# Performance work log

Measured on AMD Instinct MI355X. Metric: run time of the kernel, lower is better.

Reference implementation:

```python
import jax, jax.numpy as jnp
import numpy as np
import math

C = 256
N_HEAD = 8
GROUPS = 32
EPS = 1e-5


def group_norm(x, scale, bias, groups=GROUPS, eps=EPS):
    # x: [B, C, H, W]
    b, c, h, w = x.shape
    xg = x.reshape(b, groups, c // groups, h, w)
    mean = xg.mean(axis=(2, 3, 4), keepdims=True)
    var = xg.var(axis=(2, 3, 4), keepdims=True)
    xg = (xg - mean) * jax.lax.rsqrt(var + eps)
    x = xg.reshape(b, c, h, w)
    return x * scale[None, :, None, None] + bias[None, :, None, None]


def setup_inputs() -> dict:
    key = jax.random.key(0)
    ks = jax.random.split(key, 8)
    B, H, W = 8, 32, 32
    inp = {
        "input_q": jax.random.normal(ks[0], (B, C, H, W), dtype=jnp.float32),
        "input_kv": jax.random.normal(ks[1], (B, C, H, W), dtype=jnp.float32),
        # GroupNorm affine params (torch default: weight=1, bias=0)
        "gq_scale": jnp.ones((C,), jnp.float32),
        "gq_bias": jnp.zeros((C,), jnp.float32),
        "gkv_scale": jnp.ones((C,), jnp.float32),
        "gkv_bias": jnp.zeros((C,), jnp.float32),
        # 1x1 convs as [out, in] matrices
        "Wq": jax.random.normal(ks[2], (C, C), dtype=jnp.float32) / math.sqrt(C),
        "Wkv": jax.random.normal(ks[3], (2 * C, C), dtype=jnp.float32) / math.sqrt(C),
        "Wout": jax.random.normal(ks[4], (C, C), dtype=jnp.float32) / math.sqrt(C),
        "bout": jnp.zeros((C,), jnp.float32),
    }
    return inp


def reference(input_q, input_kv, gq_scale, gq_bias, gkv_scale, gkv_bias, Wq, Wkv, Wout, bout):
    b, c, h, w = input_q.shape
    n = N_HEAD
    d = c // n

    norm_q = group_norm(input_q, gq_scale, gq_bias)
    query = jnp.einsum('oc,bchw->bohw', Wq, norm_q).reshape(b, n, d, h, w)

    norm_kv = group_norm(input_kv, gkv_scale, gkv_bias)
    kv = jnp.einsum('oc,bchw->bohw', Wkv, norm_kv).reshape(b, n, 2 * d, h, w)
    key, value = kv[:, :, :d], kv[:, :, d:]

    attn = jnp.einsum('bnchw,bncyx->bnhwyx', query, key) / math.sqrt(c)
    attn = jax.nn.softmax(attn.reshape(b, n, h, w, h * w), axis=-1)
    attn = attn.reshape(b, n, h, w, h, w)

    out = jnp.einsum('bnhwyx,bncyx->bnchw', attn, value).reshape(b, c, h, w)
    out = jnp.einsum('oc,bchw->bohw', Wout, out) + bout[None, :, None, None]
    return out + input_q
```

## Files before the change

### kernel.cpp

```cpp
#include <hip/hip_runtime.h>
#include <hip/hip_bf16.h>
#include <math.h>
#include <string.h>

#define NB 8
#define NC 256
#define HWSZ 1024
#define NHEAD 8
#define DHEAD 32
#define NGRP 32
#define CPG 8
#define EPSV 1e-5f

typedef float f32x4 __attribute__((ext_vector_type(4)));
typedef short bf16x8 __attribute__((ext_vector_type(8)));

__device__ __forceinline__ unsigned pk2(float a, float b) {
    __hip_bfloat162 h = __float22bfloat162_rn(make_float2(a, b));
    unsigned r;
    memcpy(&r, &h, sizeof(r));
    return r;
}
__device__ __forceinline__ unsigned pk2t(float a, float b) {
    unsigned ua = __float_as_uint(a), ub = __float_as_uint(b);
    return (ua >> 16) | (ub & 0xFFFF0000u);
}
__device__ __forceinline__ unsigned short f2bf(float x) {
    __hip_bfloat16 h = __float2bfloat16(x);
    unsigned short r;
    memcpy(&r, &h, sizeof(r));
    return r;
}
__device__ __forceinline__ float ex2(float x) { return __builtin_amdgcn_exp2f(x); }

__device__ __forceinline__ void gload_lds16(const void* g, void* l) {
    __builtin_amdgcn_global_load_lds(
        (const __attribute__((address_space(1))) unsigned int*)g,
        (__attribute__((address_space(3))) unsigned int*)l, 16, 0, 0);
}

__global__ void prep_kernel(const float* __restrict__ xq,
                            const float* __restrict__ xkv,
                            const float* __restrict__ gq_scale,
                            const float* __restrict__ gq_bias,
                            const float* __restrict__ gkv_scale,
                            const float* __restrict__ gkv_bias,
                            const float* __restrict__ Wq,
                            const float* __restrict__ Wkv,
                            const float* __restrict__ Wout,
                            unsigned short* __restrict__ xnq,
                            unsigned short* __restrict__ xnkv,
                            unsigned short* __restrict__ wqb,
                            unsigned short* __restrict__ wkvb,
                            unsigned short* __restrict__ woutb) {
    if (blockIdx.x < 512) {
        int idx = blockIdx.x;
        int which = idx >> 8;
        int b = (idx >> 5) & 7;
        int g = idx & 31;
        const float* x = which ? xkv : xq;
        const float4* xb = (const float4*)(x + ((size_t)(b * NC + g * CPG)) * HWSZ);
        float s = 0.f, ss = 0.f;
        for (int i = threadIdx.x; i < (CPG * HWSZ) / 4; i += 256) {
            float4 v = xb[i];
            s += v.x + v.y + v.z + v.w;
            ss += v.x * v.x + v.y * v.y + v.z * v.z + v.w * v.w;
        }
        #pragma unroll
        for (int off = 32; off > 0; off >>= 1) {
            s += __shfl_down(s, off);
            ss += __shfl_down(ss, off);
        }
        __shared__ float red[10];
        int wid = threadIdx.x >> 6;
        if ((threadIdx.x & 63) == 0) { red[wid * 2] = s; red[wid * 2 + 1] = ss; }
        __syncthreads();
        if (threadIdx.x == 0) {
            float S = red[0] + red[2] + red[4] + red[6];
            float SS = red[1] + red[3] + red[5] + red[7];
            float mean = S * (1.f / (CPG * HWSZ));
            float var = SS * (1.f / (CPG * HWSZ)) - mean * mean;
            red[8] = mean;
            red[9] = rsqrtf(var + EPSV);
        }
        __syncthreads();
        const float mean = red[8], rstd = red[9];
        const float* scp = which ? gkv_scale : gq_scale;
        const float* bip = which ? gkv_bias : gq_bias;
        float a[8], bb[8];
        #pragma unroll
        for (int u = 0; u < 8; ++u) {
            int c = g * 8 + u;
            a[u] = rstd * scp[c];
            bb[u] = bip[c] - mean * a[u];
        }
        const int p0 = threadIdx.x * 4;
        f32x4 rowv[8];
        #pragma unroll
        for (int u = 0; u < 8; ++u)
            rowv[u] = *(const f32x4*)&x[((size_t)(b * NC + g * 8 + u)) * HWSZ + p0];
        unsigned short* xt = (which ? xnkv : xnq)
                           + (((size_t)b * NGRP + g) * HWSZ) * 8;
        #pragma unroll
        for (int pi = 0; pi < 4; ++pi) {
            uint4 o;
            o.x = pk2(rowv[0][pi] * a[0] + bb[0], rowv[1][pi] * a[1] + bb[1]);
            o.y = pk2(rowv[2][pi] * a[2] + bb[2], rowv[3][pi] * a[3] + bb[3]);
            o.z = pk2(rowv[4][pi] * a[4] + bb[4], rowv[5][pi] * a[5] + bb[5]);
            o.w = pk2(rowv[6][pi] * a[6] + bb[6], rowv[7][pi] * a[7] + bb[7]);
            *(uint4*)&xt[(size_t)(p0 + pi) * 8] = o;
        }
    } else {
        int gid = (blockIdx.x - 512) * 256 + threadIdx.x;
        int i0 = gid * 8;
        const float* src; unsigned short* dst; int off; float sc = 1.f;
        if (i0 < 65536)       { src = Wq;   dst = wqb;   off = i0;          sc = 0.0625f * 1.44269504088896f; }
        else if (i0 < 196608) { src = Wkv;  dst = wkvb;  off = i0 - 65536; }
        else                  { src = Wout; dst = woutb; off = i0 - 196608; }
        float4 v0 = *(const float4*)&src[off];
        float4 v1 = *(const float4*)&src[off + 4];
        uint4 o;
        o.x = pk2(v0.x * sc, v0.y * sc); o.y = pk2(v0.z * sc, v0.w * sc);
        o.z = pk2(v1.x * sc, v1.y * sc); o.w = pk2(v1.z * sc, v1.w * sc);
        *(uint4*)&dst[off] = o;
    }
}

__global__ __launch_bounds__(256) void qkv_gemm_kernel(
        const unsigned short* __restrict__ wqb,
        const unsigned short* __restrict__ wkvb,
        const unsigned short* __restrict__ xnq,
        const unsigned short* __restrict__ xnkv,
        unsigned short* __restrict__ qbuf,
        unsigned short* __restrict__ kbuf,
        unsigned short* __restrict__ vbuf) {
    __shared__ unsigned short Bs[64 * 256];
    const int tid = threadIdx.x;
    const int l16 = tid & 15, g = (tid >> 4) & 3, w = tid >> 6;
    const int y = blockIdx.y;
    const bool isQ = y < 4;
    const int o0 = (isQ ? y : y - 4) * 64;
    const size_t prow0 = (size_t)blockIdx.x * 64;
    const int b = (int)(prow0 >> 10);
    const int pp = (int)(prow0 & 1023);

    const unsigned short* Asrc = (isQ ? wqb : wkvb)
                               + ((size_t)o0 + 16 * w + l16) * NC;
    bf16x8 af[8];
    #pragma unroll
    for (int kk = 0; kk < 8; ++kk)
        af[kk] = *(const bf16x8*)&Asrc[(kk * 4 + g) << 3];

    const unsigned short* Xn = (isQ ? xnq : xnkv) + (size_t)b * NGRP * HWSZ * 8;
    const int prow = tid & 63, gu0 = tid >> 6;
    #pragma unroll
    for (int i = 0; i < 8; ++i) {
        int gu = gu0 + i * 4;
        uint4 v = *(const uint4*)&Xn[((size_t)gu * HWSZ + pp + prow) * 8];
        int ds = prow * 256 + ((gu ^ (prow & 7)) << 3);
        *(uint4*)&Bs[ds] = v;
    }
    __syncthreads();

    f32x4 acc[4] = {};
    const int asw = l16 & 7;
    #pragma unroll
    for (int kk = 0; kk < 8; ++kk) {
        const int koff = ((kk * 4 + g) ^ asw) << 3;
        #pragma unroll
        for (int j = 0; j < 4; ++j) {
            bf16x8 bfr = *(const bf16x8*)&Bs[(j * 16 + l16) * 256 + koff];
            acc[j] = __builtin_amdgcn_mfma_f32_16x16x32_bf16(af[kk], bfr, acc[j], 0, 0, 0);
        }
    }

    if (isQ) {
        int ob_ = o0 + 16 * w + 4 * g;
        int n = ob_ >> 5, d0 = ob_ & 31;
        unsigned short* dst = qbuf + ((size_t)(b * NHEAD + n) * HWSZ) * DHEAD + d0;
        #pragma unroll
        for (int j = 0; j < 4; ++j) {
            int p = pp + 16 * j + l16;
            uint2 st2;
            st2.x = pk2(acc[j][0], acc[j][1]);
            st2.y = pk2(acc[j][2], acc[j][3]);
            *(uint2*)&dst[(size_t)p * DHEAD] = st2;
        }
    } else {
        int n = o0 >> 6;
        int d0 = 16 * (w & 1) + 4 * g;
        if (w < 2) {
            unsigned short* dst = kbuf + ((size_t)(b * NHEAD + n) * HWSZ) * DHEAD + d0;
            #pragma unroll
            for (int j = 0; j < 4; ++j) {
                int p = pp + 16 * j + l16;
                uint2 st2;
                st2.x = pk2(acc[j][0], acc[j][1]);
                st2.y = pk2(acc[j][2], acc[j][3]);
                *(uint2*)&dst[(size_t)p * DHEAD] = st2;
            }
        } else {
            unsigned short* dst = vbuf + ((size_t)(b * NHEAD + n) * DHEAD + d0) * HWSZ;
            #pragma unroll
            for (int j = 0; j < 4; ++j) {
                int slot = ((l16 >> 2) << 3) + ((j & 1) << 2) + (l16 & 3);
                int p = pp + 32 * (j >> 1) + slot;
                #pragma unroll
                for (int r = 0; r < 4; ++r)
                    dst[(size_t)r * HWSZ + p] = f2bf(acc[j][r]);
            }
        }
    }
}

__global__ __launch_bounds__(256) void out_gemm_kernel(
        const unsigned short* __restrict__ Abase,
        const unsigned short* __restrict__ Bbase,
        const float* __restrict__ bias_out,
        const float* __restrict__ resid,
        float* __restrict__ out0) {
    __shared__ unsigned short Bs[64 * 256];
    const int tid = threadIdx.x;
    const int l16 = tid & 15, g = (tid >> 4) & 3, w = tid >> 6;
    const int o0 = blockIdx.y * 64;
    const size_t prow0 = (size_t)blockIdx.x * 64;

    const unsigned short* Asrc = Abase + (prow0 + 16 * w + l16) * NC;
    bf16x8 af[8];
    #pragma unroll
    for (int kk = 0; kk < 8; ++kk)
        af[kk] = *(const bf16x8*)&Asrc[(kk * 4 + g) << 3];

    const unsigned short* Bsrc = Bbase + (size_t)o0 * NC;
    #pragma unroll
    for (int it = 0; it < 4; ++it) {
        int idx = tid + it * 256;
        int row = idx >> 4, seg = idx & 15;
        #pragma unroll
        for (int h = 0; h < 2; ++h) {
            int sg = seg * 2 + h;
            int ds = row * 256 + ((sg ^ (row & 7)) << 3);
            *(uint4*)&Bs[ds] = *(const uint4*)&Bsrc[(size_t)row * NC + sg * 8];
        }
    }
    __syncthreads();

    f32x4 acc[4] = {};
    const int asw = l16 & 7;
    #pragma unroll
    for (int kk = 0; kk < 8; ++kk) {
        const int koff = ((kk * 4 + g) ^ asw) << 3;
        #pragma unroll
        for (int j = 0; j < 4; ++j) {
            bf16x8 b = *(const bf16x8*)&Bs[(j * 16 + l16) * 256 + koff];
            acc[j] = __builtin_amdgcn_mfma_f32_16x16x32_bf16(af[kk], b, acc[j], 0, 0, 0);
        }
    }
    const int b = (int)(prow0 >> 10);
    const int pp = (int)(prow0 & 1023);
    int p_b = pp + 16 * w + 4 * g;
    #pragma unroll
    for (int j = 0; j < 4; ++j) {
        int o = o0 + 16 * j + l16;
        float bo = bias_out[o];
        size_t off = ((size_t)b * NC + o) * HWSZ + p_b;
        float4 rs = *(const float4*)&resid[off];
        float4 vst = make_float4(acc[j][0] + bo + rs.x, acc[j][1] + bo + rs.y,
                                 acc[j][2] + bo + rs.z, acc[j][3] + bo + rs.w);
        *(float4*)&out0[off] = vst;
    }
}

__global__ __launch_bounds__(256) void attn_mfma_kernel(
        const unsigned short* __restrict__ qb,
        const unsigned short* __restrict__ kb,
        const unsigned short* __restrict__ vb,
        unsigned short* __restrict__ ob) {
    __shared__ unsigned short KV[3][4096];
    const int tid = threadIdx.x;
    const int w = tid >> 6, lane = tid & 63;
    const int l16 = lane & 15, g = lane >> 4;
    const int F = blockIdx.y * 16 + blockIdx.x;
    const int bn = (F & 7) * 8 + (F >> 7);
    const int qblk = (F >> 3) & 15;
    const int qp = qblk * 64 + w * 16 + l16;

    bf16x8 qf = *(const bf16x8*)(qb + ((size_t)bn * HWSZ + qp) * DHEAD + g * 8);

    const int kr = tid >> 2, ks = tid & 3;
    const unsigned short* ksrc = kb + (size_t)bn * HWSZ * DHEAD
                               + (size_t)kr * DHEAD + ((ks ^ (kr & 3)) << 3);
    const int vr = tid >> 3, vs = tid & 7;
    const unsigned short* vsrc = vb + (size_t)bn * DHEAD * HWSZ
                               + (size_t)vr * HWSZ + ((vs ^ (vr & 7)) << 3);
    unsigned short* lk = &KV[0][0] + w * 512;
    unsigned short* lv = &KV[0][2048] + w * 512;

#define STAGE(t) do {                                                        \
        int b3_ = (t) % 3; int ti_ = (t) & 15;                               \
        gload_lds16(ksrc + (size_t)ti_ * 64 * DHEAD, lk + b3_ * 4096);       \
        gload_lds16(vsrc + (size_t)ti_ * 64,         lv + b3_ * 4096);       \
    } while (0)

    f32x4 acc0 = {0.f, 0.f, 0.f, 0.f}, acc1 = {0.f, 0.f, 0.f, 0.f};
    f32x4 accl = {0.f, 0.f, 0.f, 0.f};
    const f32x4 z = {0.f, 0.f, 0.f, 0.f};

    const unsigned on2 = 0x3F803F80u;
    uint4 onev = make_uint4(on2, on2, on2, on2);
    bf16x8 ones;
    memcpy(&ones, &onev, sizeof(ones));

    const int ksw  = (g ^ (l16 & 3)) << 3;
    const int vsw0 = ((g)     ^ (l16 & 7)) << 3;
    const int vsw1 = ((4 + g) ^ (l16 & 7)) << 3;

    STAGE(0);
    STAGE(1);

    #pragma unroll
    for (int t = 0; t < 16; ++t) {
        const int cur = t % 3;
        asm volatile("s_waitcnt vmcnt(2)" ::: "memory");
        __builtin_amdgcn_s_barrier();
        STAGE(t + 2);

        const unsigned short* Kb = &KV[cur][0];
        const unsigned short* Vb = &KV[cur][2048];
        bf16x8 ka0 = *(const bf16x8*)&Kb[(l16)      * 32 + ksw];
        bf16x8 ka1 = *(const bf16x8*)&Kb[(16 + l16) * 32 + ksw];
        bf16x8 ka2 = *(const bf16x8*)&Kb[(32 + l16) * 32 + ksw];
        bf16x8 ka3 = *(const bf16x8*)&Kb[(48 + l16) * 32 + ksw];

        __builtin_amdgcn_s_setprio(1);
        f32x4 s0 = __builtin_amdgcn_mfma_f32_16x16x32_bf16(ka0, qf, z, 0, 0, 0);
        f32x4 s1 = __builtin_amdgcn_mfma_f32_16x16x32_bf16(ka1, qf, z, 0, 0, 0);
        f32x4 s2 = __builtin_amdgcn_mfma_f32_16x16x32_bf16(ka2, qf, z, 0, 0, 0);
        f32x4 s3 = __builtin_amdgcn_mfma_f32_16x16x32_bf16(ka3, qf, z, 0, 0, 0);
        __builtin_amdgcn_s_setprio(0);

        float p00 = ex2(s0[0]), p01 = ex2(s0[1]);
        float p02 = ex2(s0[2]), p03 = ex2(s0[3]);
        float p10 = ex2(s1[0]), p11 = ex2(s1[1]);
        float p12 = ex2(s1[2]), p13 = ex2(s1[3]);
        float p20 = ex2(s2[0]), p21 = ex2(s2[1]);
        float p22 = ex2(s2[2]), p23 = ex2(s2[3]);
        float p30 = ex2(s3[0]), p31 = ex2(s3[1]);
        float p32 = ex2(s3[2]), p33 = ex2(s3[3]);

        uint4 pwa, pwb;
        pwa.x = pk2t(p00, p01); pwa.y = pk2t(p02, p03);
        pwa.z = pk2t(p10, p11); pwa.w = pk2t(p12, p13);
        pwb.x = pk2t(p20, p21); pwb.y = pk2t(p22, p23);
        pwb.z = pk2t(p30, p31); pwb.w = pk2t(p32, p33);
        bf16x8 pf0, pf1;
        memcpy(&pf0, &pwa, sizeof(pf0));
        memcpy(&pf1, &pwb, sizeof(pf1));

        bf16x8 va0 = *(const bf16x8*)&Vb[(l16)      * 64 + vsw0];
        bf16x8 va1 = *(const bf16x8*)&Vb[(l16)      * 64 + vsw1];
        bf16x8 vb0 = *(const bf16x8*)&Vb[(16 + l16) * 64 + vsw0];
        bf16x8 vb1 = *(const bf16x8*)&Vb[(16 + l16) * 64 + vsw1];

        __builtin_amdgcn_s_setprio(1);
        acc0 = __builtin_amdgcn_mfma_f32_16x16x32_bf16(va0, pf0, acc0, 0, 0, 0);
        acc0 = __builtin_amdgcn_mfma_f32_16x16x32_bf16(va1, pf1, acc0, 0, 0, 0);
        acc1 = __builtin_amdgcn_mfma_f32_16x16x32_bf16(vb0, pf0, acc1, 0, 0, 0);
        acc1 = __builtin_amdgcn_mfma_f32_16x16x32_bf16(vb1, pf1, acc1, 0, 0, 0);
        accl = __builtin_amdgcn_mfma_f32_16x16x32_bf16(ones, pf0, accl, 0, 0, 0);
        accl = __builtin_amdgcn_mfma_f32_16x16x32_bf16(ones, pf1, accl, 0, 0, 0);
        __builtin_amdgcn_s_setprio(0);
    }
#undef STAGE

    float invl = 1.f / accl[0];

    const int b = bn >> 3, n = bn & 7;
    unsigned short* dst = ob + ((size_t)b * HWSZ + qp) * NC + n * DHEAD;
    uint2 st0, st1;
    st0.x = pk2(acc0[0] * invl, acc0[1] * invl);
    st0.y = pk2(acc0[2] * invl, acc0[3] * invl);
    st1.x = pk2(acc1[0] * invl, acc1[1] * invl);
    st1.y = pk2(acc1[2] * invl, acc1[3] * invl);
    *(uint2*)&dst[4 * g]      = st0;
    *(uint2*)&dst[16 + 4 * g] = st1;
}

extern "C" void kernel_launch(void* const* d_in, const int* in_sizes, int n_in,
                              void* d_out, int out_size, void* d_ws, size_t ws_size,
                              hipStream_t stream) {
    const float* input_q  = (const float*)d_in[0];
    const float* input_kv = (const float*)d_in[1];
    const float* gq_scale = (const float*)d_in[2];
    const float* gq_bias  = (const float*)d_in[3];
    const float* gkv_scale = (const float*)d_in[4];
    const float* gkv_bias  = (const float*)d_in[5];
    const float* Wq   = (const float*)d_in[6];
    const float* Wkv  = (const float*)d_in[7];
    const float* Wout = (const float*)d_in[8];
    const float* bout = (const float*)d_in[9];
    float* out = (float*)d_out;

    char* ws = (char*)d_ws;
    unsigned short* wqb   = (unsigned short*)(ws + 16384);
    unsigned short* wkvb  = (unsigned short*)(ws + 16384 + 131072);
    unsigned short* woutb = (unsigned short*)(ws + 16384 + 131072 + 262144);
    const size_t MB = 1024 * 1024;
    unsigned short* xnq  = (unsigned short*)(ws + 1 * MB);
    unsigned short* xnkv = (unsigned short*)(ws + 5 * MB);
    unsigned short* qbuf = (unsigned short*)(ws + 9 * MB);
    unsigned short* kbuf = (unsigned short*)(ws + 13 * MB);
    unsigned short* vbuf = (unsigned short*)(ws + 17 * MB);
    unsigned short* obuf = (unsigned short*)(ws + 21 * MB);

    prep_kernel<<<640, 256, 0, stream>>>(
        input_q, input_kv, gq_scale, gq_bias, gkv_scale, gkv_bias,
        Wq, Wkv, Wout, xnq, xnkv, wqb, wkvb, woutb);
    qkv_gemm_kernel<<<dim3(128, 12), 256, 0, stream>>>(
        wqb, wkvb, xnq, xnkv, qbuf, kbuf, vbuf);
    attn_mfma_kernel<<<dim3(16, 64), 256, 0, stream>>>(qbuf, kbuf, vbuf, obuf);
    out_gemm_kernel<<<dim3(128, 4), 256, 0, stream>>>(obuf, woutb, bout, input_q, out);
}
```

Baseline: 48.20 us.

## Switch attention kernel to 32x32x16 MFMA tiles with 128 queries per block

Rewrites the attention inner loop to use 32x32x16 bf16 MFMA instructions instead of 16x16x32. Each wave now handles 32 queries, each block 128, and the grid is halved. The K/V LDS layouts change to match the new operand fragments, and the V store order in the QKV GEMM is permuted to fit. The aim is to reuse each K/V tile across more queries and cut per-tile instruction overhead, at the cost of larger accumulators (more registers) and fewer blocks. The XOR swizzle is dropped, which may bring LDS bank conflicts.

```diff
diff --git a/kernel.cpp b/kernel.cpp
--- a/kernel.cpp
+++ b/kernel.cpp
@@ -13,6 +13,7 @@
 #define EPSV 1e-5f
 
 typedef float f32x4 __attribute__((ext_vector_type(4)));
+typedef float f32x16 __attribute__((ext_vector_type(16)));
 typedef short bf16x8 __attribute__((ext_vector_type(8)));
 
 __device__ __forceinline__ unsigned pk2(float a, float b) {
@@ -201,10 +202,10 @@
             }
         } else {
             unsigned short* dst = vbuf + ((size_t)(b * NHEAD + n) * DHEAD + d0) * HWSZ;
+            int slot = (l16 & 3) | ((l16 & 4) << 1) | ((l16 & 8) >> 1);
             #pragma unroll
             for (int j = 0; j < 4; ++j) {
-                int slot = ((l16 >> 2) << 3) + ((j & 1) << 2) + (l16 & 3);
-                int p = pp + 32 * (j >> 1) + slot;
+                int p = pp + 16 * j + slot;
                 #pragma unroll
                 for (int r = 0; r < 4; ++r)
                     dst[(size_t)r * HWSZ + p] = f2bf(acc[j][r]);
@@ -279,20 +280,21 @@
     __shared__ unsigned short KV[3][4096];
     const int tid = threadIdx.x;
     const int w = tid >> 6, lane = tid & 63;
-    const int l16 = lane & 15, g = lane >> 4;
-    const int F = blockIdx.y * 16 + blockIdx.x;
-    const int bn = (F & 7) * 8 + (F >> 7);
-    const int qblk = (F >> 3) & 15;
-    const int qp = qblk * 64 + w * 16 + l16;
-
-    bf16x8 qf = *(const bf16x8*)(qb + ((size_t)bn * HWSZ + qp) * DHEAD + g * 8);
-
-    const int kr = tid >> 2, ks = tid & 3;
+    const int l31 = lane & 31, h = lane >> 5;
+    const int F = blockIdx.y * 8 + blockIdx.x;
+    const int bn = (F & 7) * 8 + ((F >> 3) & 7);
+    const int qblk = F >> 6;
+    const int qp = qblk * 128 + w * 32 + l31;
+
+    const unsigned short* qsrc = qb + ((size_t)bn * HWSZ + qp) * DHEAD + h * 8;
+    bf16x8 qf0 = *(const bf16x8*)qsrc;
+    bf16x8 qf1 = *(const bf16x8*)(qsrc + 16);
+
     const unsigned short* ksrc = kb + (size_t)bn * HWSZ * DHEAD
-                               + (size_t)kr * DHEAD + ((ks ^ (kr & 3)) << 3);
-    const int vr = tid >> 3, vs = tid & 7;
+                               + (size_t)lane * DHEAD + w * 8;
+    const int vku = tid >> 5, vd = tid & 31;
     const unsigned short* vsrc = vb + (size_t)bn * DHEAD * HWSZ
-                               + (size_t)vr * HWSZ + ((vs ^ (vr & 7)) << 3);
+                               + (size_t)vd * HWSZ + vku * 8;
     unsigned short* lk = &KV[0][0] + w * 512;
     unsigned short* lv = &KV[0][2048] + w * 512;
 
@@ -302,18 +304,14 @@
         gload_lds16(vsrc + (size_t)ti_ * 64,         lv + b3_ * 4096);       \
     } while (0)
 
-    f32x4 acc0 = {0.f, 0.f, 0.f, 0.f}, acc1 = {0.f, 0.f, 0.f, 0.f};
-    f32x4 accl = {0.f, 0.f, 0.f, 0.f};
-    const f32x4 z = {0.f, 0.f, 0.f, 0.f};
+    f32x16 accO = {};
+    f32x16 accl = {};
+    const f32x16 z16 = {};
 
     const unsigned on2 = 0x3F803F80u;
     uint4 onev = make_uint4(on2, on2, on2, on2);
     bf16x8 ones;
     memcpy(&ones, &onev, sizeof(ones));
-
-    const int ksw  = (g ^ (l16 & 3)) << 3;
-    const int vsw0 = ((g)     ^ (l16 & 7)) << 3;
-    const int vsw1 = ((4 + g) ^ (l16 & 7)) << 3;
 
     STAGE(0);
     STAGE(1);
@@ -327,63 +325,58 @@
 
         const unsigned short* Kb = &KV[cur][0];
         const unsigned short* Vb = &KV[cur][2048];
-        bf16x8 ka0 = *(const bf16x8*)&Kb[(l16)      * 32 + ksw];
-        bf16x8 ka1 = *(const bf16x8*)&Kb[(16 + l16) * 32 + ksw];
-        bf16x8 ka2 = *(const bf16x8*)&Kb[(32 + l16) * 32 + ksw];
-        bf16x8 ka3 = *(const bf16x8*)&Kb[(48 + l16) * 32 + ksw];
-
-        __builtin_amdgcn_s_setprio(1);
-        f32x4 s0 = __builtin_amdgcn_mfma_f32_16x16x32_bf16(ka0, qf, z, 0, 0, 0);
-        f32x4 s1 = __builtin_amdgcn_mfma_f32_16x16x32_bf16(ka1, qf, z, 0, 0, 0);
-        f32x4 s2 = __builtin_amdgcn_mfma_f32_16x16x32_bf16(ka2, qf, z, 0, 0, 0);
-        f32x4 s3 = __builtin_amdgcn_mfma_f32_16x16x32_bf16(ka3, qf, z, 0, 0, 0);
-        __builtin_amdgcn_s_setprio(0);
-
-        float p00 = ex2(s0[0]), p01 = ex2(s0[1]);
-        float p02 = ex2(s0[2]), p03 = ex2(s0[3]);
-        float p10 = ex2(s1[0]), p11 = ex2(s1[1]);
-        float p12 = ex2(s1[2]), p13 = ex2(s1[3]);
-        float p20 = ex2(s2[0]), p21 = ex2(s2[1]);
-        float p22 = ex2(s2[2]), p23 = ex2(s2[3]);
-        float p30 = ex2(s3[0]), p31 = ex2(s3[1]);
-        float p32 = ex2(s3[2]), p33 = ex2(s3[3]);
-
-        uint4 pwa, pwb;
-        pwa.x = pk2t(p00, p01); pwa.y = pk2t(p02, p03);
-        pwa.z = pk2t(p10, p11); pwa.w = pk2t(p12, p13);
-        pwb.x = pk2t(p20, p21); pwb.y = pk2t(p22, p23);
-        pwb.z = pk2t(p30, p31); pwb.w = pk2t(p32, p33);
-        bf16x8 pf0, pf1;
-        memcpy(&pf0, &pwa, sizeof(pf0));
-        memcpy(&pf1, &pwb, sizeof(pf1));
-
-        bf16x8 va0 = *(const bf16x8*)&Vb[(l16)      * 64 + vsw0];
-        bf16x8 va1 = *(const bf16x8*)&Vb[(l16)      * 64 + vsw1];
-        bf16x8 vb0 = *(const bf16x8*)&Vb[(16 + l16) * 64 + vsw0];
-        bf16x8 vb1 = *(const bf16x8*)&Vb[(16 + l16) * 64 + vsw1];
-
-        __builtin_amdgcn_s_setprio(1);
-        acc0 = __builtin_amdgcn_mfma_f32_16x16x32_bf16(va0, pf0, acc0, 0, 0, 0);
-        acc0 = __builtin_amdgcn_mfma_f32_16x16x32_bf16(va1, pf1, acc0, 0, 0, 0);
-        acc1 = __builtin_amdgcn_mfma_f32_16x16x32_bf16(vb0, pf0, acc1, 0, 0, 0);
-        acc1 = __builtin_amdgcn_mfma_f32_16x16x32_bf16(vb1, pf1, acc1, 0, 0, 0);
-        accl = __builtin_amdgcn_mfma_f32_16x16x32_bf16(ones, pf0, accl, 0, 0, 0);
-        accl = __builtin_amdgcn_mfma_f32_16x16x32_bf16(ones, pf1, accl, 0, 0, 0);
-        __builtin_amdgcn_s_setprio(0);
+        bf16x8 ka00 = *(const bf16x8*)&Kb[((h)     * 64 + l31)      * 8];
+        bf16x8 ka01 = *(const bf16x8*)&Kb[((2 + h) * 64 + l31)      * 8];
+        bf16x8 ka10 = *(const bf16x8*)&Kb[((h)     * 64 + 32 + l31) * 8];
+        bf16x8 ka11 = *(const bf16x8*)&Kb[((2 + h) * 64 + 32 + l31) * 8];
+
+        f32x16 s1 = __builtin_amdgcn_mfma_f32_32x32x16_bf16(ka00, qf0, z16, 0, 0, 0);
+        s1 = __builtin_amdgcn_mfma_f32_32x32x16_bf16(ka01, qf1, s1, 0, 0, 0);
+        f32x16 s2 = __builtin_amdgcn_mfma_f32_32x32x16_bf16(ka10, qf0, z16, 0, 0, 0);
+        s2 = __builtin_amdgcn_mfma_f32_32x32x16_bf16(ka11, qf1, s2, 0, 0, 0);
+
+        uint4 pw0, pw1, pw2, pw3;
+        pw0.x = pk2t(ex2(s1[0]),  ex2(s1[1]));  pw0.y = pk2t(ex2(s1[2]),  ex2(s1[3]));
+        pw0.z = pk2t(ex2(s1[4]),  ex2(s1[5]));  pw0.w = pk2t(ex2(s1[6]),  ex2(s1[7]));
+        pw1.x = pk2t(ex2(s1[8]),  ex2(s1[9]));  pw1.y = pk2t(ex2(s1[10]), ex2(s1[11]));
+        pw1.z = pk2t(ex2(s1[12]), ex2(s1[13])); pw1.w = pk2t(ex2(s1[14]), ex2(s1[15]));
+        pw2.x = pk2t(ex2(s2[0]),  ex2(s2[1]));  pw2.y = pk2t(ex2(s2[2]),  ex2(s2[3]));
+        pw2.z = pk2t(ex2(s2[4]),  ex2(s2[5]));  pw2.w = pk2t(ex2(s2[6]),  ex2(s2[7]));
+        pw3.x = pk2t(ex2(s2[8]),  ex2(s2[9]));  pw3.y = pk2t(ex2(s2[10]), ex2(s2[11]));
+        pw3.z = pk2t(ex2(s2[12]), ex2(s2[13])); pw3.w = pk2t(ex2(s2[14]), ex2(s2[15]));
+        bf16x8 pf0, pf1, pf2, pf3;
+        memcpy(&pf0, &pw0, sizeof(pf0));
+        memcpy(&pf1, &pw1, sizeof(pf1));
+        memcpy(&pf2, &pw2, sizeof(pf2));
+        memcpy(&pf3, &pw3, sizeof(pf3));
+
+        bf16x8 va0 = *(const bf16x8*)&Vb[((0 + h) * 32 + l31) * 8];
+        bf16x8 va1 = *(const bf16x8*)&Vb[((2 + h) * 32 + l31) * 8];
+        bf16x8 va2 = *(const bf16x8*)&Vb[((4 + h) * 32 + l31) * 8];
+        bf16x8 va3 = *(const bf16x8*)&Vb[((6 + h) * 32 + l31) * 8];
+
+        accO = __builtin_amdgcn_mfma_f32_32x32x16_bf16(va0, pf0, accO, 0, 0, 0);
+        accO = __builtin_amdgcn_mfma_f32_32x32x16_bf16(va1, pf1, accO, 0, 0, 0);
+        accO = __builtin_amdgcn_mfma_f32_32x32x16_bf16(va2, pf2, accO, 0, 0, 0);
+        accO = __builtin_amdgcn_mfma_f32_32x32x16_bf16(va3, pf3, accO, 0, 0, 0);
+        accl = __builtin_amdgcn_mfma_f32_32x32x16_bf16(ones, pf0, accl, 0, 0, 0);
+        accl = __builtin_amdgcn_mfma_f32_32x32x16_bf16(ones, pf1, accl, 0, 0, 0);
+        accl = __builtin_amdgcn_mfma_f32_32x32x16_bf16(ones, pf2, accl, 0, 0, 0);
+        accl = __builtin_amdgcn_mfma_f32_32x32x16_bf16(ones, pf3, accl, 0, 0, 0);
     }
 #undef STAGE
 
     float invl = 1.f / accl[0];
 
     const int b = bn >> 3, n = bn & 7;
-    unsigned short* dst = ob + ((size_t)b * HWSZ + qp) * NC + n * DHEAD;
-    uint2 st0, st1;
-    st0.x = pk2(acc0[0] * invl, acc0[1] * invl);
-    st0.y = pk2(acc0[2] * invl, acc0[3] * invl);
-    st1.x = pk2(acc1[0] * invl, acc1[1] * invl);
-    st1.y = pk2(acc1[2] * invl, acc1[3] * invl);
-    *(uint2*)&dst[4 * g]      = st0;
-    *(uint2*)&dst[16 + 4 * g] = st1;
+    unsigned short* dst = ob + ((size_t)b * HWSZ + qp) * NC + n * DHEAD + 4 * h;
+    #pragma unroll
+    for (int gr = 0; gr < 4; ++gr) {
+        uint2 st2;
+        st2.x = pk2(accO[gr * 4 + 0] * invl, accO[gr * 4 + 1] * invl);
+        st2.y = pk2(accO[gr * 4 + 2] * invl, accO[gr * 4 + 3] * invl);
+        *(uint2*)&dst[8 * gr] = st2;
+    }
 }
 
 extern "C" void kernel_launch(void* const* d_in, const int* in_sizes, int n_in,
@@ -418,6 +411,6 @@
         Wq, Wkv, Wout, xnq, xnkv, wqb, wkvb, woutb);
     qkv_gemm_kernel<<<dim3(128, 12), 256, 0, stream>>>(
         wqb, wkvb, xnq, xnkv, qbuf, kbuf, vbuf);
-    attn_mfma_kernel<<<dim3(16, 64), 256, 0, stream>>>(qbuf, kbuf, vbuf, obuf);
+    attn_mfma_kernel<<<dim3(8, 64), 256, 0, stream>>>(qbuf, kbuf, vbuf, obuf);
     out_gemm_kernel<<<dim3(128, 4), 256, 0, stream>>>(obuf, woutb, bout, input_q, out);
 }
```

New measurement: 48.57 us. No clear change (+0.8%).
